# Performance work log

Hardware: AMD Instinct MI355X
Metric: run time of the kernel (lower is better)

## Reference

```python
import jax, jax.numpy as jnp
from jax import lax
import numpy as np

B, C, H, Wd = 32, 128, 56, 56
FILTERS = 128
KH = KW = 3
T_MIN_PREV = 0.0  # module defaults (set_params never called)
T_MIN = 0.0
T_MAX = 1.0


def setup_inputs() -> dict:
    key = jax.random.key(0)
    k1, k2 = jax.random.split(key)
    tj = jax.random.uniform(k1, (B, C, H, Wd), dtype=jnp.float32)          # spike times
    W = jax.random.normal(k2, (C * KH * KW, FILTERS), dtype=jnp.float32) * 0.02  # kernel.view(-1, filters)
    D_i = jnp.zeros((9, FILTERS), dtype=jnp.float32)                        # intrinsic delays (only row 0 used)
    return {"tj": tj, "W": W, "D_i": D_i}


def reference(tj, W, D_i):
    # 'same' padding with value t_min, then unfold + (tj - t_min) @ W is
    # exactly a zero-padded conv on (tj - t_min): the pad entries become 0.
    x = tj - T_MIN                                   # [B,C,H,W]
    # Unfold orders patch rows as (C, kh, kw); build the equivalent OIHW kernel.
    kernel = jnp.transpose(W.reshape(C, KH, KW, FILTERS), (3, 0, 1, 2))  # [F,C,KH,KW]
    y = lax.conv_general_dilated(
        x, kernel, window_strides=(1, 1), padding="SAME",
        dimension_numbers=("NCHW", "OIHW", "NCHW"))    # [B,F,H,W]
    threshold = T_MAX - T_MIN - D_i[0]                 # [F]
    ti = y + threshold[None, :, None, None] + T_MIN
    ti = jnp.minimum(ti, T_MAX)                        # torch.where(ti < t_max, ti, t_max)
    return jnp.transpose(ti, (0, 2, 3, 1))             # [B,H,W,F], matches ti.view(b,H,W,filters)
```

## Files before the change

kernel.cpp:

```cpp
#include <hip/hip_runtime.h>


#define BZ 32
#define CC 128
#define HH 56
#define WWD 56
#define HWP 3136
#define FF 128
#define PH 58
#define PW 58
#define AB_BYTES 24576
#define A_GRAN_REAL 1392
#define NSTEP 36

typedef __attribute__((ext_vector_type(8))) __bf16 bf16x8;
typedef __attribute__((ext_vector_type(4))) float f32x4;
typedef __attribute__((ext_vector_type(8))) unsigned short us8;
typedef __attribute__((ext_vector_type(4))) float flt4;

__device__ __forceinline__ unsigned short f2bf(float f) {
  unsigned int u = __float_as_uint(f);
  unsigned int r = (u + 0x7FFFu + ((u >> 16) & 1u)) >> 16;
  return (unsigned short)r;
}

#define GLOAD_LDS16(g, l)                                                              \
  __builtin_amdgcn_global_load_lds((const __attribute__((address_space(1))) void*)(g), \
                                   (__attribute__((address_space(3))) void*)(l), 16, 0, 0)

__device__ __forceinline__ int swz(int g) { return g ^ ((g >> 3) & 3); }

__global__ void prep_w_kernel(const float* __restrict__ W, unsigned short* __restrict__ Wt) {
  int idx = blockIdx.x * 256 + threadIdx.x;
  if (idx >= NSTEP * 512) return;
  int qr = idx >> 9;
  int g = idx & 511;
  int q = qr / 9, r = qr - q * 9;
  int f = g >> 2, kg = g & 3;
  us8 v;
#pragma unroll
  for (int j = 0; j < 8; ++j) {
    int c = q * 32 + kg * 8 + j;
    v[j] = f2bf(W[(c * 9 + r) * FF + f]);
  }
  *reinterpret_cast<us8*>(Wt + (size_t)idx * 8) = v;
}

__global__ __launch_bounds__(256) void prep_x_kernel(const float* __restrict__ x,
                                                     unsigned short* __restrict__ xp) {
  const int blk = blockIdx.x;
  const int b = blk / PH;
  const int ph = blk - b * PH;
  const int tid = threadIdx.x;
  unsigned short* dst = xp + (size_t)(b * PH + ph) * PW * CC;

  if (ph == 0 || ph == PH - 1) {
    us8 z;
#pragma unroll
    for (int k = 0; k < 8; ++k) z[k] = 0;
    for (int i = tid; i < PW * CC / 8; i += 256) reinterpret_cast<us8*>(dst)[i] = z;
    return;
  }

  __shared__ float sm[CC][57];
  const int h = ph - 1;
  {
    const int c = tid >> 1;
    const int half = tid & 1;
    const float* src = x + ((size_t)(b * CC + c)) * HWP + h * WWD + half * 28;
#pragma unroll
    for (int k = 0; k < 7; ++k) {
      flt4 v = *reinterpret_cast<const flt4*>(src + k * 4);
      sm[c][half * 28 + k * 4 + 0] = v[0];
      sm[c][half * 28 + k * 4 + 1] = v[1];
      sm[c][half * 28 + k * 4 + 2] = v[2];
      sm[c][half * 28 + k * 4 + 3] = v[3];
    }
  }
  __syncthreads();
  for (int i = tid; i < PW * 16; i += 256) {
    const int ww = i >> 4;
    const int cg = i & 15;
    us8 v;
    if (ww == 0 || ww == PW - 1) {
#pragma unroll
      for (int k = 0; k < 8; ++k) v[k] = 0;
    } else {
      const int w = ww - 1;
#pragma unroll
      for (int k = 0; k < 8; ++k) v[k] = f2bf(sm[cg * 8 + k][w]);
    }
    reinterpret_cast<us8*>(dst)[i] = v;
  }
}

struct Ctx {
  const unsigned short* xp;
  const unsigned short* Wt;
  int tid;
  int srcA[6];
  int gbase[7];
  int gB[4];
  f32x4 acc[7][4];
  bf16x8 bb[2][4];
};

template <int S>
__device__ __forceinline__ void step(Ctx& c, unsigned char* lds) {
  constexpr int q = S / 9, r = S - q * 9;
  const unsigned char* pa = lds + (q & 1) * AB_BYTES;

  if constexpr (S + 1 < NSTEP) {
    const unsigned short* ws = c.Wt + (size_t)(S + 1) * 4096;
#pragma unroll
    for (int j = 0; j < 4; ++j)
      c.bb[(S + 1) & 1][j] = *reinterpret_cast<const bf16x8*>(ws + c.gB[j]);
  }
  if constexpr (r == 6 && q < 3) {
#pragma unroll
    for (int k = 0; k < 6; ++k)
      GLOAD_LDS16(c.xp + c.srcA[k] + (q + 1) * 32,
                  lds + ((q + 1) & 1) * AB_BYTES + (size_t)(k * 256 + c.tid) * 16);
  }

  constexpr int dh = r / 3 - 1, dw = r - (r / 3) * 3 - 1;
  constexpr int tapoff = (dh * PW + dw) * 4;
  bf16x8 af[7];
#pragma unroll
  for (int i = 0; i < 7; ++i) {
    int gt = c.gbase[i] + tapoff;
    af[i] = *reinterpret_cast<const bf16x8*>(pa + (swz(gt) << 4));
  }

#pragma unroll
  for (int i = 0; i < 7; ++i)
#pragma unroll
    for (int j = 0; j < 4; ++j)
      c.acc[i][j] =
          __builtin_amdgcn_mfma_f32_16x16x32_bf16(af[i], c.bb[S & 1][j], c.acc[i][j], 0, 0, 0);

  if constexpr (r == 8 && q < 3) __syncthreads();
}

template <int S>
__device__ __forceinline__ void do_steps(Ctx& c, unsigned char* lds) {
  step<S>(c, lds);
  if constexpr (S + 1 < NSTEP) do_steps<S + 1>(c, lds);
}

__global__ __launch_bounds__(256, 2) void spiking_conv_main(
    const unsigned short* __restrict__ xp, const unsigned short* __restrict__ Wt,
    const float* __restrict__ Di, float* __restrict__ out) {
  __shared__ unsigned char lds[2 * AB_BYTES];

  const int bid = blockIdx.x;
  const int wg = (bid & 7) * 56 + (bid >> 3);
  const int b = wg / 14;
  const int rg = wg - b * 14;
  const int h0 = rg * 4;

  Ctx c;
  c.xp = xp;
  c.Wt = Wt;
  const int tid = threadIdx.x;
  c.tid = tid;
  const int lane = tid & 63, wv = tid >> 6;
  const int wr = wv >> 1, wc = wv & 1;
  const int frow = lane & 15, kg = lane >> 4;

#pragma unroll
  for (int k = 0; k < 6; ++k) {
    int gp = k * 256 + tid;
    int g = (gp >= A_GRAN_REAL) ? 0 : swz(gp);
    int prow = g / 232;
    int rem = g - prow * 232;
    int px = rem >> 2;
    int kg2 = rem & 3;
    c.srcA[k] = ((b * PH + h0 + prow) * PW + px) * CC + kg2 * 8;
  }
#pragma unroll
  for (int i = 0; i < 7; ++i) {
    int t = 16 * i + frow;
    int rowb = (t >= 56) ? 1 : 0;
    int col = t - 56 * rowb;
    c.gbase[i] = ((2 * wr + rowb + 1) * PW + (col + 1)) * 4 + kg;
  }
#pragma unroll
  for (int j = 0; j < 4; ++j)
    c.gB[j] = ((wc * 64 + 16 * j + frow) * 4 + kg) * 8;

  const f32x4 zero = {0.0f, 0.0f, 0.0f, 0.0f};
#pragma unroll
  for (int i = 0; i < 7; ++i)
#pragma unroll
    for (int j = 0; j < 4; ++j) c.acc[i][j] = zero;

#pragma unroll
  for (int k = 0; k < 6; ++k)
    GLOAD_LDS16(xp + c.srcA[k], lds + (size_t)(k * 256 + tid) * 16);
#pragma unroll
  for (int j = 0; j < 4; ++j)
    c.bb[0][j] = *reinterpret_cast<const bf16x8*>(Wt + c.gB[j]);
  __syncthreads();

  do_steps<0>(c, lds);

#pragma unroll
  for (int j = 0; j < 4; ++j) {
    const int col = wc * 64 + 16 * j + frow;
    const float thr = 1.0f - Di[col];
#pragma unroll
    for (int i = 0; i < 7; ++i) {
      const int bt = 16 * i + kg * 4;
      const int rowb = (bt >= 56) ? 1 : 0;
      const int wl0 = bt - 56 * rowb;
      const int orow = h0 + 2 * wr + rowb;
      const size_t obase = ((size_t)b * HWP + (size_t)orow * WWD + wl0) * FF + col;
#pragma unroll
      for (int qq = 0; qq < 4; ++qq) {
        float v = c.acc[i][j][qq] + thr;
        out[obase + (size_t)qq * FF] = fminf(v, 1.0f);
      }
    }
  }
}

__global__ __launch_bounds__(256) void spiking_conv_fallback(
    const float* __restrict__ x, const float* __restrict__ Wf,
    const float* __restrict__ Di, float* __restrict__ out) {
  __shared__ unsigned short Asm2[128][32];
  __shared__ unsigned short Bsm2[128][32];
  const int tid = threadIdx.x;
  const int m0 = blockIdx.x * 128;
  const int mi = tid & 127;
  const int half = tid >> 7;
  const int m = m0 + mi;
  const int bimg = m / HWP;
  const int p = m - bimg * HWP;
  const int h = p / WWD;
  const int w = p - h * WWD;
  const int baseA = (bimg * CC) * HWP + h * WWD + w;
  const int lane = tid & 63;
  const int wid = tid >> 6;
  const int wr = wid >> 1;
  const int wc = wid & 1;
  const int frow = lane & 15;
  const int kg = lane >> 4;
  f32x4 acc[4][4];
  const f32x4 zero = {0.0f, 0.0f, 0.0f, 0.0f};
#pragma unroll
  for (int i = 0; i < 4; ++i)
#pragma unroll
    for (int j = 0; j < 4; ++j) acc[i][j] = zero;
  for (int r = 0; r < 9; ++r) {
    const int dh = r / 3 - 1;
    const int dw = r - (r / 3) * 3 - 1;
    const int hh = h + dh;
    const int ww2 = w + dw;
    const bool valid = ((unsigned)hh < (unsigned)HH) && ((unsigned)ww2 < (unsigned)WWD);
    const int aoff2 = baseA + dh * WWD + dw + half * 16 * HWP;
    for (int c0 = 0; c0 < CC; c0 += 32) {
      __syncthreads();
      {
        const float* src = x + aoff2 + c0 * HWP;
        us8 v0, v1;
#pragma unroll
        for (int i = 0; i < 8; ++i) {
          float f0 = valid ? src[i * HWP] : 0.0f;
          float f1 = valid ? src[(i + 8) * HWP] : 0.0f;
          v0[i] = f2bf(f0);
          v1[i] = f2bf(f1);
        }
        *reinterpret_cast<us8*>(&Asm2[mi][half * 16]) = v0;
        *reinterpret_cast<us8*>(&Asm2[mi][half * 16 + 8]) = v1;
      }
      {
        us8 v0, v1;
#pragma unroll
        for (int i = 0; i < 8; ++i) {
          int cc2 = c0 + half * 16 + i;
          v0[i] = f2bf(Wf[(cc2 * 9 + r) * FF + mi]);
          v1[i] = f2bf(Wf[((cc2 + 8) * 9 + r) * FF + mi]);
        }
        *reinterpret_cast<us8*>(&Bsm2[mi][half * 16]) = v0;
        *reinterpret_cast<us8*>(&Bsm2[mi][half * 16 + 8]) = v1;
      }
      __syncthreads();
      bf16x8 af[4], bfr[4];
#pragma unroll
      for (int i = 0; i < 4; ++i)
        af[i] = *reinterpret_cast<const bf16x8*>(&Asm2[wr * 64 + i * 16 + frow][kg * 8]);
#pragma unroll
      for (int j = 0; j < 4; ++j)
        bfr[j] = *reinterpret_cast<const bf16x8*>(&Bsm2[wc * 64 + j * 16 + frow][kg * 8]);
#pragma unroll
      for (int i = 0; i < 4; ++i)
#pragma unroll
        for (int j = 0; j < 4; ++j)
          acc[i][j] = __builtin_amdgcn_mfma_f32_16x16x32_bf16(af[i], bfr[j], acc[i][j], 0, 0, 0);
    }
  }
#pragma unroll
  for (int j = 0; j < 4; ++j) {
    const int col = wc * 64 + j * 16 + frow;
    const float thr = 1.0f - Di[col];
#pragma unroll
    for (int i = 0; i < 4; ++i) {
      const int rbase = m0 + wr * 64 + i * 16 + kg * 4;
#pragma unroll
      for (int qq = 0; qq < 4; ++qq) {
        float v = acc[i][j][qq] + thr;
        out[(size_t)(rbase + qq) * FF + col] = fminf(v, 1.0f);
      }
    }
  }
}

extern "C" void kernel_launch(void* const* d_in, const int* in_sizes, int n_in,
                              void* d_out, int out_size, void* d_ws, size_t ws_size,
                              hipStream_t stream) {
  const float* tj = (const float*)d_in[0];
  const float* W = (const float*)d_in[1];
  const float* Di = (const float*)d_in[2];
  float* out = (float*)d_out;

  const size_t wt_bytes = (size_t)NSTEP * 512 * 16;
  const size_t xp_bytes = (size_t)BZ * PH * PW * CC * 2;
  unsigned short* Wt = (unsigned short*)d_ws;
  unsigned short* xp = (unsigned short*)((char*)d_ws + wt_bytes);

  bool fast = (ws_size >= wt_bytes + xp_bytes);
  if (fast) {
    prep_w_kernel<<<72, 256, 0, stream>>>(W, Wt);
    prep_x_kernel<<<BZ * PH, 256, 0, stream>>>(tj, xp);
    spiking_conv_main<<<448, 256, 0, stream>>>(xp, Wt, Di, out);
    if (hipGetLastError() != hipSuccess) fast = false;
  }
  if (!fast) {
    spiking_conv_fallback<<<100352 / 128, 256, 0, stream>>>(tj, W, Di, out);
  }
}
```

Before: 61.59 us.

## Fuse input NCHW-to-padded-bf16 conversion into main conv kernel, drop prep_x pass

Removes the separate prep_x kernel that wrote a padded NHWC bf16 copy of the input to workspace. The main conv kernel now reads fp32 NCHW rows directly, transposes them through a per-wave LDS scratch area, converts to bf16 and writes the swizzled A tile, spreading this work across steps r=1..6 of each channel quarter. This saves a full extra read/write pass over the input and one kernel launch. In exchange the conv kernel does scalar strided global loads and extra LDS traffic inside its MFMA loop, and LDS use grows to 56 KB, which may affect occupancy.

After: 83.59 us. +35.7%, slower.

```diff
diff --git a/kernel.cpp b/kernel.cpp
--- a/kernel.cpp
+++ b/kernel.cpp
@@ -10,7 +10,9 @@
 #define PH 58
 #define PW 58
 #define AB_BYTES 24576
-#define A_GRAN_REAL 1392
+#define SCR_OFF 49152
+#define SCR_WAVE 2048
+#define LDS_TOTAL 57344
 #define NSTEP 36
 
 typedef __attribute__((ext_vector_type(8))) __bf16 bf16x8;
@@ -23,10 +25,6 @@
   unsigned int r = (u + 0x7FFFu + ((u >> 16) & 1u)) >> 16;
   return (unsigned short)r;
 }
-
-#define GLOAD_LDS16(g, l)                                                              \
-  __builtin_amdgcn_global_load_lds((const __attribute__((address_space(1))) void*)(g), \
-                                   (__attribute__((address_space(3))) void*)(l), 16, 0, 0)
 
 __device__ __forceinline__ int swz(int g) { return g ^ ((g >> 3) & 3); }
 
@@ -46,65 +44,52 @@
   *reinterpret_cast<us8*>(Wt + (size_t)idx * 8) = v;
 }
 
-__global__ __launch_bounds__(256) void prep_x_kernel(const float* __restrict__ x,
-                                                     unsigned short* __restrict__ xp) {
-  const int blk = blockIdx.x;
-  const int b = blk / PH;
-  const int ph = blk - b * PH;
-  const int tid = threadIdx.x;
-  unsigned short* dst = xp + (size_t)(b * PH + ph) * PW * CC;
-
-  if (ph == 0 || ph == PH - 1) {
-    us8 z;
-#pragma unroll
-    for (int k = 0; k < 8; ++k) z[k] = 0;
-    for (int i = tid; i < PW * CC / 8; i += 256) reinterpret_cast<us8*>(dst)[i] = z;
-    return;
-  }
-
-  __shared__ float sm[CC][57];
-  const int h = ph - 1;
-  {
-    const int c = tid >> 1;
-    const int half = tid & 1;
-    const float* src = x + ((size_t)(b * CC + c)) * HWP + h * WWD + half * 28;
-#pragma unroll
-    for (int k = 0; k < 7; ++k) {
-      flt4 v = *reinterpret_cast<const flt4*>(src + k * 4);
-      sm[c][half * 28 + k * 4 + 0] = v[0];
-      sm[c][half * 28 + k * 4 + 1] = v[1];
-      sm[c][half * 28 + k * 4 + 2] = v[2];
-      sm[c][half * 28 + k * 4 + 3] = v[3];
-    }
-  }
-  __syncthreads();
-  for (int i = tid; i < PW * 16; i += 256) {
-    const int ww = i >> 4;
-    const int cg = i & 15;
-    us8 v;
-    if (ww == 0 || ww == PW - 1) {
-#pragma unroll
-      for (int k = 0; k < 8; ++k) v[k] = 0;
-    } else {
-      const int w = ww - 1;
-#pragma unroll
-      for (int k = 0; k < 8; ++k) v[k] = f2bf(sm[cg * 8 + k][w]);
-    }
-    reinterpret_cast<us8*>(dst)[i] = v;
-  }
-}
-
 struct Ctx {
-  const unsigned short* xp;
+  const float* x;
   const unsigned short* Wt;
-  int tid;
-  int srcA[6];
+  int b, h0;
+  int lane, wv;
   int gbase[7];
   int gB[4];
   f32x4 acc[7][4];
   bf16x8 bb[2][4];
 };
 
+__device__ __forceinline__ void unit(Ctx& c, unsigned char* lds, int tq, int bufpar, int u) {
+  const int cl = c.lane >> 3;
+  const int pg = c.lane & 7;
+  const int h = c.h0 + u - 1;
+  const bool rowok = ((unsigned)h < (unsigned)HH);
+
+  float* scr = reinterpret_cast<float*>(lds + SCR_OFF + c.wv * SCR_WAVE);
+
+  float v[7];
+  const float* src =
+      c.x + ((size_t)(c.b * CC + tq * 32 + c.wv * 8 + cl)) * HWP + h * WWD + pg * 7;
+#pragma unroll
+  for (int t = 0; t < 7; ++t) v[t] = rowok ? src[t] : 0.0f;
+#pragma unroll
+  for (int t = 0; t < 7; ++t) scr[(pg * 7 + t) * 8 + cl] = v[t];
+  const int p = c.lane;
+  if (p < 58) {
+    us8 g;
+    const bool gz = !rowok || p == 0 || p == 57;
+    if (gz) {
+#pragma unroll
+      for (int j = 0; j < 8; ++j) g[j] = 0;
+    } else {
+      flt4 a = *reinterpret_cast<const flt4*>(scr + (p - 1) * 8);
+      flt4 b2 = *reinterpret_cast<const flt4*>(scr + (p - 1) * 8 + 4);
+#pragma unroll
+      for (int j = 0; j < 4; ++j) g[j] = f2bf(a[j]);
+#pragma unroll
+      for (int j = 0; j < 4; ++j) g[4 + j] = f2bf(b2[j]);
+    }
+    const int gi = u * 232 + p * 4 + c.wv;
+    *reinterpret_cast<us8*>(lds + bufpar * AB_BYTES + (swz(gi) << 4)) = g;
+  }
+}
+
 template <int S>
 __device__ __forceinline__ void step(Ctx& c, unsigned char* lds) {
   constexpr int q = S / 9, r = S - q * 9;
@@ -116,11 +101,8 @@
     for (int j = 0; j < 4; ++j)
       c.bb[(S + 1) & 1][j] = *reinterpret_cast<const bf16x8*>(ws + c.gB[j]);
   }
-  if constexpr (r == 6 && q < 3) {
-#pragma unroll
-    for (int k = 0; k < 6; ++k)
-      GLOAD_LDS16(c.xp + c.srcA[k] + (q + 1) * 32,
-                  lds + ((q + 1) & 1) * AB_BYTES + (size_t)(k * 256 + c.tid) * 16);
+  if constexpr (r >= 1 && r <= 6 && q < 3) {
+    unit(c, lds, q + 1, (q + 1) & 1, r - 1);
   }
 
   constexpr int dh = r / 3 - 1, dw = r - (r / 3) * 3 - 1;
@@ -149,9 +131,9 @@
 }
 
 __global__ __launch_bounds__(256, 2) void spiking_conv_main(
-    const unsigned short* __restrict__ xp, const unsigned short* __restrict__ Wt,
+    const float* __restrict__ x, const unsigned short* __restrict__ Wt,
     const float* __restrict__ Di, float* __restrict__ out) {
-  __shared__ unsigned char lds[2 * AB_BYTES];
+  __shared__ unsigned char lds[LDS_TOTAL];
 
   const int bid = blockIdx.x;
   const int wg = (bid & 7) * 56 + (bid >> 3);
@@ -160,24 +142,17 @@
   const int h0 = rg * 4;
 
   Ctx c;
-  c.xp = xp;
+  c.x = x;
   c.Wt = Wt;
+  c.b = b;
+  c.h0 = h0;
   const int tid = threadIdx.x;
-  c.tid = tid;
   const int lane = tid & 63, wv = tid >> 6;
+  c.lane = lane;
+  c.wv = wv;
   const int wr = wv >> 1, wc = wv & 1;
   const int frow = lane & 15, kg = lane >> 4;
 
-#pragma unroll
-  for (int k = 0; k < 6; ++k) {
-    int gp = k * 256 + tid;
-    int g = (gp >= A_GRAN_REAL) ? 0 : swz(gp);
-    int prow = g / 232;
-    int rem = g - prow * 232;
-    int px = rem >> 2;
-    int kg2 = rem & 3;
-    c.srcA[k] = ((b * PH + h0 + prow) * PW + px) * CC + kg2 * 8;
-  }
 #pragma unroll
   for (int i = 0; i < 7; ++i) {
     int t = 16 * i + frow;
@@ -196,8 +171,7 @@
     for (int j = 0; j < 4; ++j) c.acc[i][j] = zero;
 
 #pragma unroll
-  for (int k = 0; k < 6; ++k)
-    GLOAD_LDS16(xp + c.srcA[k], lds + (size_t)(k * 256 + tid) * 16);
+  for (int u = 0; u < 6; ++u) unit(c, lds, 0, 0, u);
 #pragma unroll
   for (int j = 0; j < 4; ++j)
     c.bb[0][j] = *reinterpret_cast<const bf16x8*>(Wt + c.gB[j]);
@@ -325,15 +299,12 @@
   float* out = (float*)d_out;
 
   const size_t wt_bytes = (size_t)NSTEP * 512 * 16;
-  const size_t xp_bytes = (size_t)BZ * PH * PW * CC * 2;
   unsigned short* Wt = (unsigned short*)d_ws;
-  unsigned short* xp = (unsigned short*)((char*)d_ws + wt_bytes);
-
-  bool fast = (ws_size >= wt_bytes + xp_bytes);
+
+  bool fast = (ws_size >= wt_bytes);
   if (fast) {
     prep_w_kernel<<<72, 256, 0, stream>>>(W, Wt);
-    prep_x_kernel<<<BZ * PH, 256, 0, stream>>>(tj, xp);
-    spiking_conv_main<<<448, 256, 0, stream>>>(xp, Wt, Di, out);
+    spiking_conv_main<<<448, 256, 0, stream>>>(tj, Wt, Di, out);
     if (hipGetLastError() != hipSuccess) fast = false;
   }
   if (!fast) {
```
